# Kernel optimization log

Hardware: AMD Instinct MI355X
Metric: run time of the kernel (lower is better)

## Reference

```python
import jax, jax.numpy as jnp
import numpy as np

K = 3          # kernel size
PAD = 1        # padding


def _conv2d(x, w, b):
    # plain 3x3 conv, stride 1, pad 1, NCHW / OIHW
    out = jax.lax.conv_general_dilated(
        x, w, window_strides=(1, 1), padding=((PAD, PAD), (PAD, PAD)),
        dimension_numbers=('NCHW', 'OIHW', 'NCHW'))
    return out + b[None, :, None, None]


def _deform_conv2d(x, offsets, w, b):
    # torchvision deform_conv2d semantics (stride=1, dilation=1, no mask)
    B, C, H, W = x.shape
    K2 = K * K
    off = offsets.reshape(B, K2, 2, H, W)
    dy, dx = off[:, :, 0], off[:, :, 1]              # [B,K2,H,W], (y,x) order
    ki, kj = jnp.meshgrid(jnp.arange(K), jnp.arange(K), indexing='ij')
    ki = ki.reshape(K2).astype(x.dtype)
    kj = kj.reshape(K2).astype(x.dtype)
    base_y = (jnp.arange(H, dtype=x.dtype)[None, :, None] - PAD + ki[:, None, None])  # [K2,H,1]
    base_x = (jnp.arange(W, dtype=x.dtype)[None, None, :] - PAD + kj[:, None, None])  # [K2,1,W]
    py = base_y[None] + dy                            # [B,K2,H,W] sampling rows
    px = base_x[None] + dx                            # [B,K2,H,W] sampling cols

    y0 = jnp.floor(py); x0 = jnp.floor(px)
    y1 = y0 + 1.0;      x1 = x0 + 1.0
    wy1 = py - y0; wy0 = 1.0 - wy1
    wx1 = px - x0; wx0 = 1.0 - wx1

    def corner(yc, xc, wgt):
        valid = ((yc >= 0) & (yc <= H - 1) & (xc >= 0) & (xc <= W - 1))
        iy = jnp.clip(yc, 0, H - 1).astype(jnp.int32)
        ix = jnp.clip(xc, 0, W - 1).astype(jnp.int32)
        # per-batch gather: x[b][:, iy[b], ix[b]] -> [C,K2,H,W]
        vals = jax.vmap(lambda xb, iyb, ixb: xb[:, iyb, ixb])(x, iy, ix)
        return vals * (wgt * valid.astype(x.dtype))[:, None]  # [B,C,K2,H,W]

    sampled = (corner(y0, x0, wy0 * wx0) + corner(y0, x1, wy0 * wx1)
               + corner(y1, x0, wy1 * wx0) + corner(y1, x1, wy1 * wx1))
    out = jnp.einsum('bckhw,ock->bohw', sampled, w.reshape(w.shape[0], C, K2))
    return out + b[None, :, None, None]


def setup_inputs() -> dict:
    key = jax.random.key(0)
    ks = jax.random.split(key, 6)
    B, C, O, H, W = 4, 256, 256, 64, 64
    x = jax.random.normal(ks[0], (B, C, H, W), dtype=jnp.float32)
    y = jax.random.normal(ks[1], (B, C, H, W), dtype=jnp.float32)
    # offset conv predicts 2*K*K offset channels; small init keeps offsets a few px
    offset_w = jax.random.normal(ks[2], (2 * K * K, C, K, K), dtype=jnp.float32) * 0.01
    offset_b = jax.random.normal(ks[3], (2 * K * K,), dtype=jnp.float32) * 0.01
    deform_w = jax.random.normal(ks[4], (O, C, K, K), dtype=jnp.float32) * (1.0 / np.sqrt(C * K * K))
    deform_b = jax.random.normal(ks[5], (O,), dtype=jnp.float32) * 0.01
    return {"x": x, "y": y, "offset_w": offset_w, "offset_b": offset_b,
            "deform_w": deform_w, "deform_b": deform_b}


def reference(x, y, offset_w, offset_b, deform_w, deform_b):
    offsets = _conv2d(y, offset_w, offset_b)          # [B, 2*K*K, H, W]
    return _deform_conv2d(x, offsets, deform_w, deform_b)
```

## Files before the change

kernel.cpp:

```cpp
#include <hip/hip_runtime.h>
#include <hip/hip_bf16.h>
#include <stdint.h>


typedef __bf16 bf16x8 __attribute__((ext_vector_type(8)));
typedef float  f32x4  __attribute__((ext_vector_type(4)));

__device__ __forceinline__ unsigned short f2bfu(float f) {
    union { float f; unsigned u; } v; v.f = f;
    return (unsigned short)((v.u + 0x8000u) >> 16);
}
__device__ __forceinline__ float lo16(unsigned u) {
    union { unsigned u; float f; } v; v.u = u << 16; return v.f;
}
__device__ __forceinline__ float hi16(unsigned u) {
    union { unsigned u; float f; } v; v.u = u & 0xFFFF0000u; return v.f;
}
__device__ __forceinline__ unsigned fbits(float f) {
    union { float f; unsigned u; } v; v.f = f; return v.u;
}
__device__ __forceinline__ unsigned blend2(unsigned u0, unsigned u1, unsigned u2, unsigned u3,
                                           float4 w) {
    float lo = w.x * lo16(u0) + w.y * lo16(u1) + w.z * lo16(u2) + w.w * lo16(u3);
    float hi = w.x * hi16(u0) + w.y * hi16(u1) + w.z * hi16(u2) + w.w * hi16(u3);
    unsigned rl = fbits(lo) + 0x8000u;
    unsigned rh = fbits(hi) + 0x8000u;
    return __builtin_amdgcn_perm(rh, rl, 0x07060302);
}

__global__ __launch_bounds__(256) void prep_kernel(
    const float* __restrict__ x, const float* __restrict__ y,
    const float* __restrict__ ow, const float* __restrict__ dw,
    unsigned short* __restrict__ xT, unsigned short* __restrict__ yT,
    unsigned short* __restrict__ Wp2, unsigned short* __restrict__ Bo)
{
    __shared__ float tile[64 * 69];
    int blk = blockIdx.x;
    int t = threadIdx.x;
    if (blk < 2048) {
        const float* src = x; unsigned short* dst = xT;
        if (blk >= 1024) { src = y; dst = yT; blk -= 1024; }
        int cq = blk & 3;
        int bh = blk >> 2;
        int w4 = t & 15, cl0 = t >> 4;
        const float* s = src + ((size_t)(bh >> 6) * 256 + cq * 64) * 4096 + (size_t)(bh & 63) * 64;
#pragma unroll
        for (int p = 0; p < 4; ++p) {
            int cl = p * 16 + cl0;
            float4 v = *(const float4*)&s[(size_t)cl * 4096 + w4 * 4];
            tile[(w4 * 4 + 0) * 69 + cl] = v.x;
            tile[(w4 * 4 + 1) * 69 + cl] = v.y;
            tile[(w4 * 4 + 2) * 69 + cl] = v.z;
            tile[(w4 * 4 + 3) * 69 + cl] = v.w;
        }
        __syncthreads();
        unsigned short* d = dst + (size_t)bh * 16384 + cq * 64;
#pragma unroll
        for (int p = 0; p < 4; ++p) {
            int w = p * 16 + cl0;
            float4 v = *(const float4*)&tile[w * 69 + w4 * 4];
            ushort4 r = make_ushort4(f2bfu(v.x), f2bfu(v.y), f2bfu(v.z), f2bfu(v.w));
            *(ushort4*)&d[w * 256 + w4 * 4] = r;
        }
    } else if (blk < 2336) {
        int tid = (blk - 2048) * 256 + t;
        int q8 = tid >> 8;
        int o  = tid & 255;
        int k0 = q8 * 8;
        int tap = k0 >> 8, c0 = k0 & 255;
        const float* s = dw + o * 2304 + c0 * 9 + tap;
        ushort4 r0 = make_ushort4(f2bfu(s[0]), f2bfu(s[9]), f2bfu(s[18]), f2bfu(s[27]));
        ushort4 r1 = make_ushort4(f2bfu(s[36]), f2bfu(s[45]), f2bfu(s[54]), f2bfu(s[63]));
        *(ushort4*)&Wp2[tid * 8 + 0] = r0;
        *(ushort4*)&Wp2[tid * 8 + 4] = r1;
    } else {
        int idx = (blk - 2336) * 256 + t;
        int j = idx & 7;
        int n = (idx >> 3) & 31;
        int lq = (idx >> 8) & 3;
        int kg = idx >> 10;
        int k = kg * 32 + lq * 8 + j;
        int tap = k >> 8, c = k & 255;
        float v = (n < 18) ? ow[n * 2304 + c * 9 + tap] : 0.f;
        Bo[idx] = f2bfu(v);
    }
}

__global__ __launch_bounds__(1024) void deform_kernel(
    const unsigned short* __restrict__ xT,
    const unsigned short* __restrict__ yT,
    const unsigned short* __restrict__ Wp2,
    const unsigned short* __restrict__ Bo,
    const float* __restrict__ ob,
    const float* __restrict__ db,
    float* __restrict__ out)
{
    __shared__ __align__(16) unsigned char smem[88064];
    unsigned short* Abuf0 = (unsigned short*)smem;
    unsigned short* Abuf1 = (unsigned short*)(smem + 32768);
    float*  red = (float*)smem;
    float*  epi = (float*)smem;
    float4* pw_lds = (float4*)(smem + 69632);
    int4*   pi_lds = (int4*)(smem + 69632 + 9216);

    int blk = blockIdx.x;
    int lb = (blk & 7) * 32 + (blk >> 3);
    int b = lb >> 6, h = lb & 63;
    int t = threadIdx.x;
    int wv = t >> 6, lane = t & 63;
    int ln = lane & 15, lq = lane >> 4;

    const unsigned short* xtb = xT + (size_t)b * (64 * 64 * 256);

    {
        int kq = wv >> 1, mh = wv & 1;
        f32x4 oacc[2][2];
#pragma unroll
        for (int m16 = 0; m16 < 2; ++m16)
#pragma unroll
            for (int nt = 0; nt < 2; ++nt)
                oacc[m16][nt] = (f32x4){0.f, 0.f, 0.f, 0.f};
        for (int u = kq * 9; u < kq * 9 + 9; ++u) {
            int tap = u >> 3, kc = u & 7;
            int ki = tap / 3, kj = tap - ki * 3;
            int hr = h + ki - 1;
            bf16x8 b0 = *(const bf16x8*)&Bo[(tap * 8 + kc) * 1024 + lq * 256 + ln * 8];
            bf16x8 b1 = *(const bf16x8*)&Bo[(tap * 8 + kc) * 1024 + lq * 256 + (16 + ln) * 8];
#pragma unroll
            for (int m16 = 0; m16 < 2; ++m16) {
                int wr = mh * 32 + m16 * 16 + ln + kj - 1;
                bf16x8 af = (bf16x8)(__bf16)0.0f;
                if (hr >= 0 && hr < 64 && wr >= 0 && wr < 64)
                    af = *(const bf16x8*)&yT[((size_t)(b * 64 + hr) * 64 + wr) * 256 + kc * 32 + lq * 8];
                oacc[m16][0] = __builtin_amdgcn_mfma_f32_16x16x32_bf16(af, b0, oacc[m16][0], 0, 0, 0);
                oacc[m16][1] = __builtin_amdgcn_mfma_f32_16x16x32_bf16(af, b1, oacc[m16][1], 0, 0, 0);
            }
        }
        float* rz = red + (size_t)(kq * 2 + mh) * 1056;
#pragma unroll
        for (int m16 = 0; m16 < 2; ++m16)
#pragma unroll
            for (int nt = 0; nt < 2; ++nt) {
                int o_l = nt * 16 + ln;
#pragma unroll
                for (int r = 0; r < 4; ++r)
                    rz[o_l * 33 + m16 * 16 + lq * 4 + r] = oacc[m16][nt][r];
            }
    }
    __syncthreads();
    if (t < 576) {
        int tap = t >> 6, pos = t & 63;
        int mh_p = pos >> 5, pl = pos & 31;
        float dy = ob[2 * tap], dx = ob[2 * tap + 1];
#pragma unroll
        for (int kq = 0; kq < 8; ++kq) {
            const float* rz = red + (size_t)(kq * 2 + mh_p) * 1056;
            dy += rz[(2 * tap) * 33 + pl];
            dx += rz[(2 * tap + 1) * 33 + pl];
        }
        int ki = tap / 3, kj = tap - ki * 3;
        float py = (float)(h - 1 + ki) + dy;
        float px = (float)(pos - 1 + kj) + dx;
        float y0 = floorf(py), x0 = floorf(px);
        float wy1 = py - y0, wx1 = px - x0;
        float wy0 = 1.f - wy1, wx0 = 1.f - wx1;
        float y1 = y0 + 1.f, x1 = x0 + 1.f;
        float vy0 = (y0 >= 0.f && y0 <= 63.f) ? 1.f : 0.f;
        float vy1 = (y1 >= 0.f && y1 <= 63.f) ? 1.f : 0.f;
        float vx0 = (x0 >= 0.f && x0 <= 63.f) ? 1.f : 0.f;
        float vx1 = (x1 >= 0.f && x1 <= 63.f) ? 1.f : 0.f;
        int iy0 = (int)fminf(fmaxf(y0, 0.f), 63.f);
        int iy1 = (int)fminf(fmaxf(y1, 0.f), 63.f);
        int ix0 = (int)fminf(fmaxf(x0, 0.f), 63.f);
        int ix1 = (int)fminf(fmaxf(x1, 0.f), 63.f);
        pw_lds[t] = make_float4(wy0 * wx0 * vy0 * vx0, wy0 * wx1 * vy0 * vx1,
                                wy1 * wx0 * vy1 * vx0, wy1 * wx1 * vy1 * vx1);
        pi_lds[t] = make_int4((iy0 * 64 + ix0) * 256, (iy0 * 64 + ix1) * 256,
                              (iy1 * 64 + ix0) * 256, (iy1 * 64 + ix1) * 256);
    }
    __syncthreads();

    int ns = wv & 7, kh = wv >> 3;

    f32x4 acc[4][2];
#pragma unroll
    for (int ms = 0; ms < 4; ++ms)
#pragma unroll
        for (int nt = 0; nt < 2; ++nt)
            acc[ms][nt] = (f32x4){0.f, 0.f, 0.f, 0.f};

    int gr = t & 31, c0 = gr * 8;
    uint4 ga[2][4]; float4 gw[2];
#pragma unroll
    for (int it = 0; it < 2; ++it) {
        int pos = (t >> 5) + it * 32;
        gw[it] = pw_lds[pos];
        int4 p = pi_lds[pos];
        ga[it][0] = *(const uint4*)&xtb[p.x + c0];
        ga[it][1] = *(const uint4*)&xtb[p.y + c0];
        ga[it][2] = *(const uint4*)&xtb[p.z + c0];
        ga[it][3] = *(const uint4*)&xtb[p.w + c0];
    }
#pragma unroll
    for (int it = 0; it < 2; ++it) {
        int pos = (t >> 5) + it * 32;
        uint4 res;
        res.x = blend2(ga[it][0].x, ga[it][1].x, ga[it][2].x, ga[it][3].x, gw[it]);
        res.y = blend2(ga[it][0].y, ga[it][1].y, ga[it][2].y, ga[it][3].y, gw[it]);
        res.z = blend2(ga[it][0].z, ga[it][1].z, ga[it][2].z, ga[it][3].z, gw[it]);
        res.w = blend2(ga[it][0].w, ga[it][1].w, ga[it][2].w, ga[it][3].w, gw[it]);
        *(uint4*)&Abuf0[pos * 256 + (gr ^ (pos & 7)) * 8] = res;
    }
    __syncthreads();

    for (int tap = 0; tap < 9; ++tap) {
        if (tap < 8) {
#pragma unroll
            for (int it = 0; it < 2; ++it) {
                int pos = (t >> 5) + it * 32;
                gw[it] = pw_lds[(tap + 1) * 64 + pos];
                int4 p = pi_lds[(tap + 1) * 64 + pos];
                ga[it][0] = *(const uint4*)&xtb[p.x + c0];
                ga[it][1] = *(const uint4*)&xtb[p.y + c0];
                ga[it][2] = *(const uint4*)&xtb[p.z + c0];
                ga[it][3] = *(const uint4*)&xtb[p.w + c0];
            }
        }
        const unsigned short* Ab = (tap & 1) ? Abuf1 : Abuf0;
#pragma unroll
        for (int kc = 0; kc < 4; ++kc) {
            int gbase = kh * 16 + kc * 4 + lq;
            bf16x8 af[4];
#pragma unroll
            for (int ms = 0; ms < 4; ++ms) {
                int row = ms * 16 + ln;
                af[ms] = *(const bf16x8*)&Ab[row * 256 + (gbase ^ (row & 7)) * 8];
            }
            int kg = tap * 8 + kh * 4 + kc;
            bf16x8 bfr[2];
#pragma unroll
            for (int nt = 0; nt < 2; ++nt)
                bfr[nt] = *(const bf16x8*)&Wp2[((kg * 4 + lq) * 256 + ns * 32 + nt * 16 + ln) * 8];
#pragma unroll
            for (int ms = 0; ms < 4; ++ms)
#pragma unroll
                for (int nt = 0; nt < 2; ++nt)
                    acc[ms][nt] = __builtin_amdgcn_mfma_f32_16x16x32_bf16(af[ms], bfr[nt], acc[ms][nt], 0, 0, 0);
        }
        if (tap < 8) {
            unsigned short* buf = (tap & 1) ? Abuf0 : Abuf1;
#pragma unroll
            for (int it = 0; it < 2; ++it) {
                int pos = (t >> 5) + it * 32;
                uint4 res;
                res.x = blend2(ga[it][0].x, ga[it][1].x, ga[it][2].x, ga[it][3].x, gw[it]);
                res.y = blend2(ga[it][0].y, ga[it][1].y, ga[it][2].y, ga[it][3].y, gw[it]);
                res.z = blend2(ga[it][0].z, ga[it][1].z, ga[it][2].z, ga[it][3].z, gw[it]);
                res.w = blend2(ga[it][0].w, ga[it][1].w, ga[it][2].w, ga[it][3].w, gw[it]);
                *(uint4*)&buf[pos * 256 + (gr ^ (pos & 7)) * 8] = res;
            }
        }
        __syncthreads();
    }

    if (kh == 1) {
        float* e = epi + (size_t)ns * 2176;
#pragma unroll
        for (int ms = 0; ms < 4; ++ms)
#pragma unroll
            for (int nt = 0; nt < 2; ++nt) {
                int o_l = nt * 16 + ln;
                f32x4 a = acc[ms][nt];
                *(float4*)&e[o_l * 68 + ms * 16 + lq * 4] = make_float4(a[0], a[1], a[2], a[3]);
            }
    }
    __syncthreads();
    if (kh == 0) {
        const float* e = epi + (size_t)ns * 2176;
#pragma unroll
        for (int ms = 0; ms < 4; ++ms)
#pragma unroll
            for (int nt = 0; nt < 2; ++nt) {
                int o_l = nt * 16 + ln;
                int o = ns * 32 + o_l;
                float bias = db[o];
                float4 p = *(const float4*)&e[o_l * 68 + ms * 16 + lq * 4];
                f32x4 a = acc[ms][nt];
                float4 st = make_float4(a[0] + p.x + bias, a[1] + p.y + bias,
                                        a[2] + p.z + bias, a[3] + p.w + bias);
                *(float4*)&out[((size_t)(b * 256 + o)) * 4096 + h * 64 + ms * 16 + lq * 4] = st;
            }
    }
}

extern "C" void kernel_launch(void* const* d_in, const int* in_sizes, int n_in,
                              void* d_out, int out_size, void* d_ws, size_t ws_size,
                              hipStream_t stream) {
    const float* x  = (const float*)d_in[0];
    const float* y  = (const float*)d_in[1];
    const float* ow = (const float*)d_in[2];
    const float* ob = (const float*)d_in[3];
    const float* dw = (const float*)d_in[4];
    const float* db = (const float*)d_in[5];
    float* out = (float*)d_out;

    char* ws = (char*)d_ws;
    unsigned short* xT  = (unsigned short*)(ws);
    unsigned short* yT  = (unsigned short*)(ws + 8388608);
    unsigned short* Wp2 = (unsigned short*)(ws + 16777216);
    unsigned short* Bo  = (unsigned short*)(ws + 16777216 + 1179648);

    hipLaunchKernelGGL(prep_kernel, dim3(2624), dim3(256), 0, stream,
                       x, y, ow, dw, xT, yT, Wp2, Bo);
    hipLaunchKernelGGL(deform_kernel, dim3(256), dim3(1024), 0, stream,
                       xT, yT, Wp2, Bo, ob, db, out);
}
```

Measured before the change: 136.5 us.

## Quad-buffer gathered A tiles and halve barriers in deform conv tap loop

Replaces the double-buffered LDS staging of the bilinear-gathered activation tiles with a four-slot ring, processing two taps per barrier so only five block-wide syncs remain instead of nine. Gather loads for the next tap are issued before each MFMA block, with sched_barrier to keep them ahead and s_setprio raised around the MFMA section. This aims to cut barrier stalls and hide global gather latency behind matrix work. It raises LDS use to about 146 KB per block.

```diff
diff --git a/kernel.cpp b/kernel.cpp
--- a/kernel.cpp
+++ b/kernel.cpp
@@ -86,6 +86,70 @@
     }
 }
 
+
+struct GatherRegs { uint4 ga[2][4]; float4 gw[2]; };
+
+__device__ __forceinline__ void issue_tap(GatherRegs& G, int tap, int t,
+                                          const unsigned short* __restrict__ xtb, int c0,
+                                          const float4* __restrict__ pw_lds,
+                                          const int4* __restrict__ pi_lds)
+{
+#pragma unroll
+    for (int it = 0; it < 2; ++it) {
+        int pos = (t >> 5) + it * 32;
+        G.gw[it] = pw_lds[tap * 64 + pos];
+        int4 p = pi_lds[tap * 64 + pos];
+        G.ga[it][0] = *(const uint4*)&xtb[p.x + c0];
+        G.ga[it][1] = *(const uint4*)&xtb[p.y + c0];
+        G.ga[it][2] = *(const uint4*)&xtb[p.z + c0];
+        G.ga[it][3] = *(const uint4*)&xtb[p.w + c0];
+    }
+}
+
+__device__ __forceinline__ void commit_tap(const GatherRegs& G, unsigned short* buf,
+                                           int t, int gr)
+{
+#pragma unroll
+    for (int it = 0; it < 2; ++it) {
+        int pos = (t >> 5) + it * 32;
+        uint4 res;
+        res.x = blend2(G.ga[it][0].x, G.ga[it][1].x, G.ga[it][2].x, G.ga[it][3].x, G.gw[it]);
+        res.y = blend2(G.ga[it][0].y, G.ga[it][1].y, G.ga[it][2].y, G.ga[it][3].y, G.gw[it]);
+        res.z = blend2(G.ga[it][0].z, G.ga[it][1].z, G.ga[it][2].z, G.ga[it][3].z, G.gw[it]);
+        res.w = blend2(G.ga[it][0].w, G.ga[it][1].w, G.ga[it][2].w, G.ga[it][3].w, G.gw[it]);
+        *(uint4*)&buf[pos * 256 + (gr ^ (pos & 7)) * 8] = res;
+    }
+}
+
+__device__ __forceinline__ void mfma_tap(f32x4 (&acc)[4][2],
+                                         const unsigned short* __restrict__ Ab,
+                                         const unsigned short* __restrict__ Wp2,
+                                         int tap, int kh, int lq, int ln, int ns)
+{
+    __builtin_amdgcn_s_setprio(1);
+#pragma unroll
+    for (int kc = 0; kc < 4; ++kc) {
+        int gbase = kh * 16 + kc * 4 + lq;
+        bf16x8 af[4];
+#pragma unroll
+        for (int ms = 0; ms < 4; ++ms) {
+            int row = ms * 16 + ln;
+            af[ms] = *(const bf16x8*)&Ab[row * 256 + (gbase ^ (row & 7)) * 8];
+        }
+        int kg = tap * 8 + kh * 4 + kc;
+        bf16x8 bfr[2];
+#pragma unroll
+        for (int nt = 0; nt < 2; ++nt)
+            bfr[nt] = *(const bf16x8*)&Wp2[((kg * 4 + lq) * 256 + ns * 32 + nt * 16 + ln) * 8];
+#pragma unroll
+        for (int ms = 0; ms < 4; ++ms)
+#pragma unroll
+            for (int nt = 0; nt < 2; ++nt)
+                acc[ms][nt] = __builtin_amdgcn_mfma_f32_16x16x32_bf16(af[ms], bfr[nt], acc[ms][nt], 0, 0, 0);
+    }
+    __builtin_amdgcn_s_setprio(0);
+}
+
 __global__ __launch_bounds__(1024) void deform_kernel(
     const unsigned short* __restrict__ xT,
     const unsigned short* __restrict__ yT,
@@ -95,13 +159,12 @@
     const float* __restrict__ db,
     float* __restrict__ out)
 {
-    __shared__ __align__(16) unsigned char smem[88064];
-    unsigned short* Abuf0 = (unsigned short*)smem;
-    unsigned short* Abuf1 = (unsigned short*)(smem + 32768);
+    __shared__ __align__(16) unsigned char smem[149504];
+    unsigned short* Abase = (unsigned short*)smem;
     float*  red = (float*)smem;
     float*  epi = (float*)smem;
-    float4* pw_lds = (float4*)(smem + 69632);
-    int4*   pi_lds = (int4*)(smem + 69632 + 9216);
+    float4* pw_lds = (float4*)(smem + 131072);
+    int4*   pi_lds = (int4*)(smem + 131072 + 9216);
 
     int blk = blockIdx.x;
     int lb = (blk & 7) * 32 + (blk >> 3);
@@ -190,78 +253,32 @@
             acc[ms][nt] = (f32x4){0.f, 0.f, 0.f, 0.f};
 
     int gr = t & 31, c0 = gr * 8;
-    uint4 ga[2][4]; float4 gw[2];
-#pragma unroll
-    for (int it = 0; it < 2; ++it) {
-        int pos = (t >> 5) + it * 32;
-        gw[it] = pw_lds[pos];
-        int4 p = pi_lds[pos];
-        ga[it][0] = *(const uint4*)&xtb[p.x + c0];
-        ga[it][1] = *(const uint4*)&xtb[p.y + c0];
-        ga[it][2] = *(const uint4*)&xtb[p.z + c0];
-        ga[it][3] = *(const uint4*)&xtb[p.w + c0];
-    }
-#pragma unroll
-    for (int it = 0; it < 2; ++it) {
-        int pos = (t >> 5) + it * 32;
-        uint4 res;
-        res.x = blend2(ga[it][0].x, ga[it][1].x, ga[it][2].x, ga[it][3].x, gw[it]);
-        res.y = blend2(ga[it][0].y, ga[it][1].y, ga[it][2].y, ga[it][3].y, gw[it]);
-        res.z = blend2(ga[it][0].z, ga[it][1].z, ga[it][2].z, ga[it][3].z, gw[it]);
-        res.w = blend2(ga[it][0].w, ga[it][1].w, ga[it][2].w, ga[it][3].w, gw[it]);
-        *(uint4*)&Abuf0[pos * 256 + (gr ^ (pos & 7)) * 8] = res;
-    }
-    __syncthreads();
-
-    for (int tap = 0; tap < 9; ++tap) {
-        if (tap < 8) {
-#pragma unroll
-            for (int it = 0; it < 2; ++it) {
-                int pos = (t >> 5) + it * 32;
-                gw[it] = pw_lds[(tap + 1) * 64 + pos];
-                int4 p = pi_lds[(tap + 1) * 64 + pos];
-                ga[it][0] = *(const uint4*)&xtb[p.x + c0];
-                ga[it][1] = *(const uint4*)&xtb[p.y + c0];
-                ga[it][2] = *(const uint4*)&xtb[p.z + c0];
-                ga[it][3] = *(const uint4*)&xtb[p.w + c0];
-            }
-        }
-        const unsigned short* Ab = (tap & 1) ? Abuf1 : Abuf0;
-#pragma unroll
-        for (int kc = 0; kc < 4; ++kc) {
-            int gbase = kh * 16 + kc * 4 + lq;
-            bf16x8 af[4];
-#pragma unroll
-            for (int ms = 0; ms < 4; ++ms) {
-                int row = ms * 16 + ln;
-                af[ms] = *(const bf16x8*)&Ab[row * 256 + (gbase ^ (row & 7)) * 8];
-            }
-            int kg = tap * 8 + kh * 4 + kc;
-            bf16x8 bfr[2];
-#pragma unroll
-            for (int nt = 0; nt < 2; ++nt)
-                bfr[nt] = *(const bf16x8*)&Wp2[((kg * 4 + lq) * 256 + ns * 32 + nt * 16 + ln) * 8];
-#pragma unroll
-            for (int ms = 0; ms < 4; ++ms)
-#pragma unroll
-                for (int nt = 0; nt < 2; ++nt)
-                    acc[ms][nt] = __builtin_amdgcn_mfma_f32_16x16x32_bf16(af[ms], bfr[nt], acc[ms][nt], 0, 0, 0);
-        }
-        if (tap < 8) {
-            unsigned short* buf = (tap & 1) ? Abuf0 : Abuf1;
-#pragma unroll
-            for (int it = 0; it < 2; ++it) {
-                int pos = (t >> 5) + it * 32;
-                uint4 res;
-                res.x = blend2(ga[it][0].x, ga[it][1].x, ga[it][2].x, ga[it][3].x, gw[it]);
-                res.y = blend2(ga[it][0].y, ga[it][1].y, ga[it][2].y, ga[it][3].y, gw[it]);
-                res.z = blend2(ga[it][0].z, ga[it][1].z, ga[it][2].z, ga[it][3].z, gw[it]);
-                res.w = blend2(ga[it][0].w, ga[it][1].w, ga[it][2].w, ga[it][3].w, gw[it]);
-                *(uint4*)&buf[pos * 256 + (gr ^ (pos & 7)) * 8] = res;
-            }
-        }
+    GatherRegs G;
+
+    issue_tap(G, 0, t, xtb, c0, pw_lds, pi_lds);
+    commit_tap(G, Abase + 0 * 16384, t, gr);
+    issue_tap(G, 1, t, xtb, c0, pw_lds, pi_lds);
+    commit_tap(G, Abase + 1 * 16384, t, gr);
+    __syncthreads();
+
+    for (int i = 0; i < 4; ++i) {
+        int tp0 = 2 * i, tp1 = 2 * i + 1;
+        int s0 = tp0 + 2, s1 = tp1 + 2;
+        issue_tap(G, s0, t, xtb, c0, pw_lds, pi_lds);
+        __builtin_amdgcn_sched_barrier(0);
+        mfma_tap(acc, Abase + (tp0 & 3) * 16384, Wp2, tp0, kh, lq, ln, ns);
+        commit_tap(G, Abase + (s0 & 3) * 16384, t, gr);
+        if (s1 < 9) {
+            issue_tap(G, s1, t, xtb, c0, pw_lds, pi_lds);
+            __builtin_amdgcn_sched_barrier(0);
+        }
+        mfma_tap(acc, Abase + (tp1 & 3) * 16384, Wp2, tp1, kh, lq, ln, ns);
+        if (s1 < 9)
+            commit_tap(G, Abase + (s1 & 3) * 16384, t, gr);
         __syncthreads();
     }
+    mfma_tap(acc, Abase + 0 * 16384, Wp2, 8, kh, lq, ln, ns);
+    __syncthreads();
 
     if (kh == 1) {
         float* e = epi + (size_t)ns * 2176;
```

New measurement: 131.0 us. 4.0% less time.

## Halve deform block to 512 threads, drop split-K reduction, use hardware bf16 pack

Applied to the files above, without the earlier changes.

The deform kernel moves from 1024 to 512 threads per block. Each wave now covers the full K range for its 32 output channels, so the LDS split-K epilogue reduction and its extra barrier go away. Each thread gathers four positions per tap instead of two, the offset-conv phase gives each wave both halves of the row, and the MFMA loop is fenced with sched_barrier and setprio. The bf16 rounding-plus-perm sequence becomes a single v_cvt_pk_bf16_f32. The cost is more registers per thread and less parallelism per block; launch_bounds(512,2) asks for two blocks per CU, but with about 86 KB of LDS per block that may not be reachable, and the grid is only 256 blocks anyway.

```diff
diff --git a/kernel.cpp b/kernel.cpp
--- a/kernel.cpp
+++ b/kernel.cpp
@@ -16,16 +16,16 @@
 __device__ __forceinline__ float hi16(unsigned u) {
     union { unsigned u; float f; } v; v.u = u & 0xFFFF0000u; return v.f;
 }
-__device__ __forceinline__ unsigned fbits(float f) {
-    union { float f; unsigned u; } v; v.f = f; return v.u;
+__device__ __forceinline__ unsigned cvtpk_bf16(float lo, float hi) {
+    unsigned r;
+    asm("v_cvt_pk_bf16_f32 %0, %1, %2" : "=v"(r) : "v"(lo), "v"(hi));
+    return r;
 }
 __device__ __forceinline__ unsigned blend2(unsigned u0, unsigned u1, unsigned u2, unsigned u3,
                                            float4 w) {
     float lo = w.x * lo16(u0) + w.y * lo16(u1) + w.z * lo16(u2) + w.w * lo16(u3);
     float hi = w.x * hi16(u0) + w.y * hi16(u1) + w.z * hi16(u2) + w.w * hi16(u3);
-    unsigned rl = fbits(lo) + 0x8000u;
-    unsigned rh = fbits(hi) + 0x8000u;
-    return __builtin_amdgcn_perm(rh, rl, 0x07060302);
+    return cvtpk_bf16(lo, hi);
 }
 
 __global__ __launch_bounds__(256) void prep_kernel(
@@ -86,7 +86,7 @@
     }
 }
 
-__global__ __launch_bounds__(1024) void deform_kernel(
+__global__ __launch_bounds__(512, 2) void deform_kernel(
     const unsigned short* __restrict__ xT,
     const unsigned short* __restrict__ yT,
     const unsigned short* __restrict__ Wp2,
@@ -95,13 +95,12 @@
     const float* __restrict__ db,
     float* __restrict__ out)
 {
-    __shared__ __align__(16) unsigned char smem[88064];
-    unsigned short* Abuf0 = (unsigned short*)smem;
-    unsigned short* Abuf1 = (unsigned short*)(smem + 32768);
+    __shared__ __align__(16) unsigned char smem[86016];
+    unsigned short* Ab0 = (unsigned short*)smem;
+    unsigned short* Ab1 = (unsigned short*)(smem + 32768);
     float*  red = (float*)smem;
-    float*  epi = (float*)smem;
-    float4* pw_lds = (float4*)(smem + 69632);
-    int4*   pi_lds = (int4*)(smem + 69632 + 9216);
+    float4* pw_lds = (float4*)(smem + 67584);
+    int4*   pi_lds = (int4*)(smem + 67584 + 9216);
 
     int blk = blockIdx.x;
     int lb = (blk & 7) * 32 + (blk >> 3);
@@ -113,13 +112,15 @@
     const unsigned short* xtb = xT + (size_t)b * (64 * 64 * 256);
 
     {
-        int kq = wv >> 1, mh = wv & 1;
-        f32x4 oacc[2][2];
-#pragma unroll
-        for (int m16 = 0; m16 < 2; ++m16)
-#pragma unroll
-            for (int nt = 0; nt < 2; ++nt)
-                oacc[m16][nt] = (f32x4){0.f, 0.f, 0.f, 0.f};
+        int kq = wv;
+        f32x4 oacc[2][2][2];
+#pragma unroll
+        for (int mh = 0; mh < 2; ++mh)
+#pragma unroll
+            for (int m16 = 0; m16 < 2; ++m16)
+#pragma unroll
+                for (int nt = 0; nt < 2; ++nt)
+                    oacc[mh][m16][nt] = (f32x4){0.f, 0.f, 0.f, 0.f};
         for (int u = kq * 9; u < kq * 9 + 9; ++u) {
             int tap = u >> 3, kc = u & 7;
             int ki = tap / 3, kj = tap - ki * 3;
@@ -127,29 +128,34 @@
             bf16x8 b0 = *(const bf16x8*)&Bo[(tap * 8 + kc) * 1024 + lq * 256 + ln * 8];
             bf16x8 b1 = *(const bf16x8*)&Bo[(tap * 8 + kc) * 1024 + lq * 256 + (16 + ln) * 8];
 #pragma unroll
-            for (int m16 = 0; m16 < 2; ++m16) {
-                int wr = mh * 32 + m16 * 16 + ln + kj - 1;
-                bf16x8 af = (bf16x8)(__bf16)0.0f;
-                if (hr >= 0 && hr < 64 && wr >= 0 && wr < 64)
-                    af = *(const bf16x8*)&yT[((size_t)(b * 64 + hr) * 64 + wr) * 256 + kc * 32 + lq * 8];
-                oacc[m16][0] = __builtin_amdgcn_mfma_f32_16x16x32_bf16(af, b0, oacc[m16][0], 0, 0, 0);
-                oacc[m16][1] = __builtin_amdgcn_mfma_f32_16x16x32_bf16(af, b1, oacc[m16][1], 0, 0, 0);
-            }
-        }
-        float* rz = red + (size_t)(kq * 2 + mh) * 1056;
-#pragma unroll
-        for (int m16 = 0; m16 < 2; ++m16)
-#pragma unroll
-            for (int nt = 0; nt < 2; ++nt) {
-                int o_l = nt * 16 + ln;
-#pragma unroll
-                for (int r = 0; r < 4; ++r)
-                    rz[o_l * 33 + m16 * 16 + lq * 4 + r] = oacc[m16][nt][r];
-            }
+            for (int mh = 0; mh < 2; ++mh)
+#pragma unroll
+                for (int m16 = 0; m16 < 2; ++m16) {
+                    int wr = mh * 32 + m16 * 16 + ln + kj - 1;
+                    bf16x8 af = (bf16x8)(__bf16)0.0f;
+                    if (hr >= 0 && hr < 64 && wr >= 0 && wr < 64)
+                        af = *(const bf16x8*)&yT[((size_t)(b * 64 + hr) * 64 + wr) * 256 + kc * 32 + lq * 8];
+                    oacc[mh][m16][0] = __builtin_amdgcn_mfma_f32_16x16x32_bf16(af, b0, oacc[mh][m16][0], 0, 0, 0);
+                    oacc[mh][m16][1] = __builtin_amdgcn_mfma_f32_16x16x32_bf16(af, b1, oacc[mh][m16][1], 0, 0, 0);
+                }
+        }
+#pragma unroll
+        for (int mh = 0; mh < 2; ++mh) {
+            float* rz = red + (size_t)(kq * 2 + mh) * 1056;
+#pragma unroll
+            for (int m16 = 0; m16 < 2; ++m16)
+#pragma unroll
+                for (int nt = 0; nt < 2; ++nt) {
+                    int o_l = nt * 16 + ln;
+#pragma unroll
+                    for (int r = 0; r < 4; ++r)
+                        rz[o_l * 33 + m16 * 16 + lq * 4 + r] = oacc[mh][m16][nt][r];
+                }
+        }
     }
     __syncthreads();
-    if (t < 576) {
-        int tap = t >> 6, pos = t & 63;
+    for (int j = t; j < 576; j += 512) {
+        int tap = j >> 6, pos = j & 63;
         int mh_p = pos >> 5, pl = pos & 31;
         float dy = ob[2 * tap], dx = ob[2 * tap + 1];
 #pragma unroll
@@ -173,14 +179,16 @@
         int iy1 = (int)fminf(fmaxf(y1, 0.f), 63.f);
         int ix0 = (int)fminf(fmaxf(x0, 0.f), 63.f);
         int ix1 = (int)fminf(fmaxf(x1, 0.f), 63.f);
-        pw_lds[t] = make_float4(wy0 * wx0 * vy0 * vx0, wy0 * wx1 * vy0 * vx1,
+        pw_lds[j] = make_float4(wy0 * wx0 * vy0 * vx0, wy0 * wx1 * vy0 * vx1,
                                 wy1 * wx0 * vy1 * vx0, wy1 * wx1 * vy1 * vx1);
-        pi_lds[t] = make_int4((iy0 * 64 + ix0) * 256, (iy0 * 64 + ix1) * 256,
+        pi_lds[j] = make_int4((iy0 * 64 + ix0) * 256, (iy0 * 64 + ix1) * 256,
                               (iy1 * 64 + ix0) * 256, (iy1 * 64 + ix1) * 256);
     }
     __syncthreads();
 
-    int ns = wv & 7, kh = wv >> 3;
+    int ns = wv;
+    int gr = t & 31, c0 = gr * 8;
+    int pbase = t >> 5;
 
     f32x4 acc[4][2];
 #pragma unroll
@@ -189,35 +197,37 @@
         for (int nt = 0; nt < 2; ++nt)
             acc[ms][nt] = (f32x4){0.f, 0.f, 0.f, 0.f};
 
-    int gr = t & 31, c0 = gr * 8;
-    uint4 ga[2][4]; float4 gw[2];
-#pragma unroll
-    for (int it = 0; it < 2; ++it) {
-        int pos = (t >> 5) + it * 32;
-        gw[it] = pw_lds[pos];
-        int4 p = pi_lds[pos];
-        ga[it][0] = *(const uint4*)&xtb[p.x + c0];
-        ga[it][1] = *(const uint4*)&xtb[p.y + c0];
-        ga[it][2] = *(const uint4*)&xtb[p.z + c0];
-        ga[it][3] = *(const uint4*)&xtb[p.w + c0];
-    }
-#pragma unroll
-    for (int it = 0; it < 2; ++it) {
-        int pos = (t >> 5) + it * 32;
-        uint4 res;
-        res.x = blend2(ga[it][0].x, ga[it][1].x, ga[it][2].x, ga[it][3].x, gw[it]);
-        res.y = blend2(ga[it][0].y, ga[it][1].y, ga[it][2].y, ga[it][3].y, gw[it]);
-        res.z = blend2(ga[it][0].z, ga[it][1].z, ga[it][2].z, ga[it][3].z, gw[it]);
-        res.w = blend2(ga[it][0].w, ga[it][1].w, ga[it][2].w, ga[it][3].w, gw[it]);
-        *(uint4*)&Abuf0[pos * 256 + (gr ^ (pos & 7)) * 8] = res;
+    {
+        uint4 ga[4][4]; float4 gw[4];
+#pragma unroll
+        for (int it = 0; it < 4; ++it) {
+            int pos = pbase + it * 16;
+            gw[it] = pw_lds[pos];
+            int4 p = pi_lds[pos];
+            ga[it][0] = *(const uint4*)&xtb[p.x + c0];
+            ga[it][1] = *(const uint4*)&xtb[p.y + c0];
+            ga[it][2] = *(const uint4*)&xtb[p.z + c0];
+            ga[it][3] = *(const uint4*)&xtb[p.w + c0];
+        }
+#pragma unroll
+        for (int it = 0; it < 4; ++it) {
+            int pos = pbase + it * 16;
+            uint4 res;
+            res.x = blend2(ga[it][0].x, ga[it][1].x, ga[it][2].x, ga[it][3].x, gw[it]);
+            res.y = blend2(ga[it][0].y, ga[it][1].y, ga[it][2].y, ga[it][3].y, gw[it]);
+            res.z = blend2(ga[it][0].z, ga[it][1].z, ga[it][2].z, ga[it][3].z, gw[it]);
+            res.w = blend2(ga[it][0].w, ga[it][1].w, ga[it][2].w, ga[it][3].w, gw[it]);
+            *(uint4*)&Ab0[pos * 256 + (gr ^ (pos & 7)) * 8] = res;
+        }
     }
     __syncthreads();
 
     for (int tap = 0; tap < 9; ++tap) {
+        uint4 ga[4][4]; float4 gw[4];
         if (tap < 8) {
 #pragma unroll
-            for (int it = 0; it < 2; ++it) {
-                int pos = (t >> 5) + it * 32;
+            for (int it = 0; it < 4; ++it) {
+                int pos = pbase + it * 16;
                 gw[it] = pw_lds[(tap + 1) * 64 + pos];
                 int4 p = pi_lds[(tap + 1) * 64 + pos];
                 ga[it][0] = *(const uint4*)&xtb[p.x + c0];
@@ -226,32 +236,38 @@
                 ga[it][3] = *(const uint4*)&xtb[p.w + c0];
             }
         }
-        const unsigned short* Ab = (tap & 1) ? Abuf1 : Abuf0;
-#pragma unroll
-        for (int kc = 0; kc < 4; ++kc) {
-            int gbase = kh * 16 + kc * 4 + lq;
-            bf16x8 af[4];
-#pragma unroll
-            for (int ms = 0; ms < 4; ++ms) {
-                int row = ms * 16 + ln;
-                af[ms] = *(const bf16x8*)&Ab[row * 256 + (gbase ^ (row & 7)) * 8];
+        __builtin_amdgcn_sched_barrier(0);
+        {
+            const unsigned short* Ab = (tap & 1) ? Ab1 : Ab0;
+            __builtin_amdgcn_s_setprio(1);
+#pragma unroll
+            for (int kc = 0; kc < 8; ++kc) {
+                int gbase = kc * 4 + lq;
+                bf16x8 af[4];
+#pragma unroll
+                for (int ms = 0; ms < 4; ++ms) {
+                    int row = ms * 16 + ln;
+                    af[ms] = *(const bf16x8*)&Ab[row * 256 + (gbase ^ (row & 7)) * 8];
+                }
+                int kg = tap * 8 + kc;
+                bf16x8 bfr[2];
+#pragma unroll
+                for (int nt = 0; nt < 2; ++nt)
+                    bfr[nt] = *(const bf16x8*)&Wp2[((kg * 4 + lq) * 256 + ns * 32 + nt * 16 + ln) * 8];
+#pragma unroll
+                for (int ms = 0; ms < 4; ++ms)
+#pragma unroll
+                    for (int nt = 0; nt < 2; ++nt)
+                        acc[ms][nt] = __builtin_amdgcn_mfma_f32_16x16x32_bf16(af[ms], bfr[nt], acc[ms][nt], 0, 0, 0);
             }
-            int kg = tap * 8 + kh * 4 + kc;
-            bf16x8 bfr[2];
-#pragma unroll
-            for (int nt = 0; nt < 2; ++nt)
-                bfr[nt] = *(const bf16x8*)&Wp2[((kg * 4 + lq) * 256 + ns * 32 + nt * 16 + ln) * 8];
-#pragma unroll
-            for (int ms = 0; ms < 4; ++ms)
-#pragma unroll
-                for (int nt = 0; nt < 2; ++nt)
-                    acc[ms][nt] = __builtin_amdgcn_mfma_f32_16x16x32_bf16(af[ms], bfr[nt], acc[ms][nt], 0, 0, 0);
-        }
+            __builtin_amdgcn_s_setprio(0);
+        }
+        __builtin_amdgcn_sched_barrier(0);
         if (tap < 8) {
-            unsigned short* buf = (tap & 1) ? Abuf0 : Abuf1;
-#pragma unroll
-            for (int it = 0; it < 2; ++it) {
-                int pos = (t >> 5) + it * 32;
+            unsigned short* buf = (tap & 1) ? Ab0 : Ab1;
+#pragma unroll
+            for (int it = 0; it < 4; ++it) {
+                int pos = pbase + it * 16;
                 uint4 res;
                 res.x = blend2(ga[it][0].x, ga[it][1].x, ga[it][2].x, ga[it][3].x, gw[it]);
                 res.y = blend2(ga[it][0].y, ga[it][1].y, ga[it][2].y, ga[it][3].y, gw[it]);
@@ -263,34 +279,16 @@
         __syncthreads();
     }
 
-    if (kh == 1) {
-        float* e = epi + (size_t)ns * 2176;
-#pragma unroll
-        for (int ms = 0; ms < 4; ++ms)
-#pragma unroll
-            for (int nt = 0; nt < 2; ++nt) {
-                int o_l = nt * 16 + ln;
-                f32x4 a = acc[ms][nt];
-                *(float4*)&e[o_l * 68 + ms * 16 + lq * 4] = make_float4(a[0], a[1], a[2], a[3]);
-            }
-    }
-    __syncthreads();
-    if (kh == 0) {
-        const float* e = epi + (size_t)ns * 2176;
-#pragma unroll
-        for (int ms = 0; ms < 4; ++ms)
-#pragma unroll
-            for (int nt = 0; nt < 2; ++nt) {
-                int o_l = nt * 16 + ln;
-                int o = ns * 32 + o_l;
-                float bias = db[o];
-                float4 p = *(const float4*)&e[o_l * 68 + ms * 16 + lq * 4];
-                f32x4 a = acc[ms][nt];
-                float4 st = make_float4(a[0] + p.x + bias, a[1] + p.y + bias,
-                                        a[2] + p.z + bias, a[3] + p.w + bias);
-                *(float4*)&out[((size_t)(b * 256 + o)) * 4096 + h * 64 + ms * 16 + lq * 4] = st;
-            }
-    }
+#pragma unroll
+    for (int ms = 0; ms < 4; ++ms)
+#pragma unroll
+        for (int nt = 0; nt < 2; ++nt) {
+            int o = ns * 32 + nt * 16 + ln;
+            float bias = db[o];
+            f32x4 a = acc[ms][nt];
+            float4 st = make_float4(a[0] + bias, a[1] + bias, a[2] + bias, a[3] + bias);
+            *(float4*)&out[((size_t)(b * 256 + o)) * 4096 + h * 64 + ms * 16 + lq * 4] = st;
+        }
 }
 
 extern "C" void kernel_launch(void* const* d_in, const int* in_sizes, int n_in,
@@ -312,6 +310,6 @@
 
     hipLaunchKernelGGL(prep_kernel, dim3(2624), dim3(256), 0, stream,
                        x, y, ow, dw, xT, yT, Wp2, Bo);
-    hipLaunchKernelGGL(deform_kernel, dim3(256), dim3(1024), 0, stream,
+    hipLaunchKernelGGL(deform_kernel, dim3(256), dim3(512), 0, stream,
                        xT, yT, Wp2, Bo, ob, db, out);
 }
```

Result: slower. 148.0 us (+8.4%).
